# Kernel optimization log

Measured on AMD Instinct MI355X. Metric: run time of the kernel, lower is better.

Reference implementation:

```python
import jax, jax.numpy as jnp
import numpy as np

B, D_IN, D_PROJ, N_CLS = 4096, 4096, 1024, 32
N_CHILD = (32, 64)


def setup_inputs() -> dict:
    key = jax.random.key(0)
    ks = jax.random.split(key, 12)
    std = 2e-05
    inp = {
        "x": jax.random.normal(ks[0], (B, D_IN), dtype=jnp.float32),
        "y": jax.random.randint(ks[1], (B,), 0, N_CLS, dtype=jnp.int32),
        # parent projection: Linear(D_IN, D_PROJ)
        "Wp": jax.random.normal(ks[2], (D_IN, D_PROJ), dtype=jnp.float32) * std,
        "bp": jnp.zeros((D_PROJ,), jnp.float32),
        # subclass projection: Linear(D_IN, D_PROJ)
        "Ws": jax.random.normal(ks[3], (D_IN, D_PROJ), dtype=jnp.float32) * std,
        "bs": jnp.zeros((D_PROJ,), jnp.float32),
        # parent classifier: Linear(D_PROJ, N_CLS)
        "Wc": jax.random.normal(ks[4], (D_PROJ, N_CLS), dtype=jnp.float32) * std,
        "bc": jnp.zeros((N_CLS,), jnp.float32),
        # child expert banks: level i has N_CLS experts of Linear(D_PROJ, N_CHILD[i])
        "cw0": jax.random.normal(ks[5], (N_CLS, N_CHILD[0], D_PROJ), dtype=jnp.float32) * std,
        "cb0": jnp.zeros((N_CLS, N_CHILD[0]), jnp.float32),
        "cw1": jax.random.normal(ks[6], (N_CLS, N_CHILD[1], D_PROJ), dtype=jnp.float32) * std,
        "cb1": jnp.zeros((N_CLS, N_CHILD[1]), jnp.float32),
    }
    return inp


def reference(x, y, Wp, bp, Ws, bs, Wc, bc, cw0, cb0, cw1, cb1):
    # dropout p = 0.0 -> identity
    parent_proj_embed = x @ Wp + bp                 # [B, D_PROJ]
    parent_logits = parent_proj_embed @ Wc + bc     # [B, N_CLS]
    child_proj_embed = x @ Ws + bs                  # [B, D_PROJ]
    # per-sample expert routing: gather the expert for label y[b], then batched matvec
    child_logits0 = jnp.einsum("bd,bnd->bn", child_proj_embed, cw0[y]) + cb0[y]  # [B, 32]
    child_logits1 = jnp.einsum("bd,bnd->bn", child_proj_embed, cw1[y]) + cb1[y]  # [B, 64]
    return (parent_logits, child_logits0, child_logits1, parent_proj_embed, child_proj_embed)
```

## Files before the change

kernel.cpp:

```cpp
#include <hip/hip_runtime.h>
#include <hip/hip_bf16.h>
#include <stdint.h>


typedef __attribute__((ext_vector_type(4))) float  floatx4;
typedef __attribute__((ext_vector_type(8))) short  shortx8;
typedef __attribute__((ext_vector_type(4))) short  shortx4;
typedef __attribute__((ext_vector_type(8))) __bf16 bf16x8;

static __device__ __forceinline__ ushort f32_to_bf16_rne(float f) {
  uint32_t u = __builtin_bit_cast(uint32_t, f);
  u += 0x7FFFu + ((u >> 16) & 1u);
  return (ushort)(u >> 16);
}

static __device__ __forceinline__ void async_copy16(const void* g, void* lds) {
  __builtin_amdgcn_global_load_lds(
      (__attribute__((address_space(1))) void*)(uintptr_t)g,
      (__attribute__((address_space(3))) void*)(uintptr_t)lds,
      16, 0, 0);
}

__global__ __launch_bounds__(256) void k_prep(
    const float* __restrict__ x,   const int* __restrict__ y,
    const float* __restrict__ Wp,  const float* __restrict__ Ws,
    const float* __restrict__ Wc,
    const float* __restrict__ cw0, const float* __restrict__ cw1,
    ushort* __restrict__ xb,  ushort* __restrict__ Bt1,
    ushort* __restrict__ cwb, ushort* __restrict__ Wcb,
    int* __restrict__ perm, int* __restrict__ offs)
{
  __shared__ __align__(16) ushort tile[64 * 72];
  __shared__ int hist[32], hbase[32], hcur[32];
  const int b = blockIdx.x;
  const int t = threadIdx.x;

  if (b == 0) {
    if (t < 32) { hist[t] = 0; hcur[t] = 0; }
    __syncthreads();
    int yv[16];
    #pragma unroll
    for (int i = 0; i < 16; ++i) { yv[i] = y[t * 16 + i]; atomicAdd(&hist[yv[i]], 1); }
    __syncthreads();
    if (t == 0) {
      int s = 0;
      for (int c = 0; c < 32; ++c) { hbase[c] = s; offs[c] = s; s += hist[c]; }
      offs[32] = s;
    }
    __syncthreads();
    #pragma unroll
    for (int i = 0; i < 16; ++i) {
      const int c = yv[i];
      const int p = atomicAdd(&hcur[c], 1);
      perm[hbase[c] + p] = t * 16 + i;
    }
  } else if (b <= 4224) {
    const int row = b - 1;
    const int k = t * 4;
    float v0 = 0.f, v1 = 0.f, v2 = 0.f, v3 = 0.f;
    ushort* dst;
    if (row < 4096) {
      const int c = row >> 7, n = row & 127;
      if (n < 32) {
        floatx4 f = *reinterpret_cast<const floatx4*>(cw0 + (size_t)(c * 32 + n) * 1024 + k);
        v0 = f[0]; v1 = f[1]; v2 = f[2]; v3 = f[3];
      } else if (n < 96) {
        floatx4 f = *reinterpret_cast<const floatx4*>(cw1 + (size_t)(c * 64 + (n - 32)) * 1024 + k);
        v0 = f[0]; v1 = f[1]; v2 = f[2]; v3 = f[3];
      }
      dst = cwb + (size_t)row * 1024 + k;
    } else {
      const int n = row - 4096;
      if (n < 32) {
        v0 = Wc[(k + 0) * 32 + n]; v1 = Wc[(k + 1) * 32 + n];
        v2 = Wc[(k + 2) * 32 + n]; v3 = Wc[(k + 3) * 32 + n];
      }
      dst = Wcb + (size_t)n * 1024 + k;
    }
    shortx4 o;
    o[0] = (short)f32_to_bf16_rne(v0); o[1] = (short)f32_to_bf16_rne(v1);
    o[2] = (short)f32_to_bf16_rne(v2); o[3] = (short)f32_to_bf16_rne(v3);
    *reinterpret_cast<shortx4*>(dst) = o;
  } else if (b <= 6272) {
    const int vt = b - 4225;
    const int z = vt >> 10, rest = vt & 1023;
    const int nt = rest >> 6, kt = rest & 63;
    const float* W = z ? Ws : Wp;
    const int r = t >> 4, c = (t & 15) * 4;
    #pragma unroll
    for (int j = 0; j < 4; ++j) {
      const int kk = r + j * 16;
      floatx4 v = *reinterpret_cast<const floatx4*>(
          W + (size_t)(kt * 64 + kk) * 1024 + nt * 64 + c);
      tile[(c + 0) * 72 + kk] = f32_to_bf16_rne(v[0]);
      tile[(c + 1) * 72 + kk] = f32_to_bf16_rne(v[1]);
      tile[(c + 2) * 72 + kk] = f32_to_bf16_rne(v[2]);
      tile[(c + 3) * 72 + kk] = f32_to_bf16_rne(v[3]);
    }
    __syncthreads();
    const int nl = t >> 3, ch = t & 7;
    #pragma unroll
    for (int j = 0; j < 2; ++j) {
      const int n = nl + j * 32;
      shortx8 v = *reinterpret_cast<const shortx8*>(tile + n * 72 + ch * 8);
      *reinterpret_cast<shortx8*>(
          Bt1 + (size_t)(z * 1024 + nt * 64 + n) * 4096 + kt * 64 + ch * 8) = v;
    }
  } else {
    const size_t i = ((size_t)(b - 6273) * 256 + t) * 8;
    floatx4 a = *reinterpret_cast<const floatx4*>(x + i);
    floatx4 c = *reinterpret_cast<const floatx4*>(x + i + 4);
    shortx8 o;
    o[0] = (short)f32_to_bf16_rne(a[0]); o[1] = (short)f32_to_bf16_rne(a[1]);
    o[2] = (short)f32_to_bf16_rne(a[2]); o[3] = (short)f32_to_bf16_rne(a[3]);
    o[4] = (short)f32_to_bf16_rne(c[0]); o[5] = (short)f32_to_bf16_rne(c[1]);
    o[6] = (short)f32_to_bf16_rne(c[2]); o[7] = (short)f32_to_bf16_rne(c[3]);
    *reinterpret_cast<shortx8*>(xb + i) = o;
  }
}

__global__ __launch_bounds__(512, 2) void k_gemm1(
    const ushort* __restrict__ xb, const ushort* __restrict__ Bt1,
    const float* __restrict__ bp, const float* __restrict__ bs,
    float* __restrict__ outP, float* __restrict__ outS,
    ushort* __restrict__ Pb, ushort* __restrict__ Sb)
{
  __shared__ __align__(16) ushort lA[3 * 256 * 64];
  __shared__ __align__(16) ushort lB[3 * 128 * 64];

  floatx4 acc[4][4];
  const floatx4 z4 = {0.f, 0.f, 0.f, 0.f};
  #pragma unroll
  for (int i = 0; i < 4; ++i)
    #pragma unroll
    for (int j = 0; j < 4; ++j) acc[i][j] = z4;

  const int t    = threadIdx.x;
  const int w    = t >> 6;
  const int lane = t & 63;
  const int wr   = w >> 1;
  const int wc   = w & 1;
  const int r16  = lane & 15;
  const int qd   = lane >> 4;

  const ushort* Abase = xb  + (size_t)(blockIdx.x * 256) * 4096;
  const ushort* Bbase = Bt1 + (size_t)(blockIdx.y * 128) * 4096;

  const int    rS   = t >> 3;
  const int    qs   = ((t & 7) ^ (rS & 7)) << 3;
  const int    dUni = (t & ~63) * 8;

  const int px0 = (0 * 4 + qd) ^ (r16 & 7);
  const int px1 = (1 * 4 + qd) ^ (r16 & 7);
  const int aRd = (wr * 64 + r16) * 64;
  const int bRd = (wc * 64 + r16) * 64;

  #define STAGE_CHUNK(slot, k0)                                                \
    do {                                                                       \
      _Pragma("unroll")                                                        \
      for (int j = 0; j < 4; ++j)                                              \
        async_copy16(Abase + (size_t)(j * 64 + rS) * 4096 + (k0) + qs,         \
                     lA + (slot) * 16384 + j * 4096 + dUni);                   \
      _Pragma("unroll")                                                        \
      for (int j = 0; j < 2; ++j)                                              \
        async_copy16(Bbase + (size_t)(j * 64 + rS) * 4096 + (k0) + qs,         \
                     lB + (slot) * 8192 + j * 4096 + dUni);                    \
    } while (0)

  STAGE_CHUNK(0, 0);
  STAGE_CHUNK(1, 64);
  asm volatile("s_waitcnt vmcnt(6)" ::: "memory");
  __builtin_amdgcn_s_barrier();
  asm volatile("" ::: "memory");

  for (int c = 0; c < 64; ++c) {
    const int slot = c % 3;
    const ushort* As = lA + slot * 16384;
    const ushort* Bs = lB + slot * 8192;

    bf16x8 af[2][4], bfv[2][4];
    #pragma unroll
    for (int mi = 0; mi < 4; ++mi) {
      af[0][mi] = *reinterpret_cast<const bf16x8*>(As + aRd + mi * 1024 + px0 * 8);
      af[1][mi] = *reinterpret_cast<const bf16x8*>(As + aRd + mi * 1024 + px1 * 8);
    }
    #pragma unroll
    for (int ni = 0; ni < 4; ++ni) {
      bfv[0][ni] = *reinterpret_cast<const bf16x8*>(Bs + bRd + ni * 1024 + px0 * 8);
      bfv[1][ni] = *reinterpret_cast<const bf16x8*>(Bs + bRd + ni * 1024 + px1 * 8);
    }

    {
      const int cs  = c + 2;
      const int ss  = cs % 3;
      const int k0s = (cs < 64 ? cs : 63) * 64;
      STAGE_CHUNK(ss, k0s);
    }

    __builtin_amdgcn_s_setprio(1);
    #pragma unroll
    for (int ks = 0; ks < 2; ++ks)
      #pragma unroll
      for (int mi = 0; mi < 4; ++mi)
        #pragma unroll
        for (int ni = 0; ni < 4; ++ni)
          acc[mi][ni] = __builtin_amdgcn_mfma_f32_16x16x32_bf16(
              af[ks][mi], bfv[ks][ni], acc[mi][ni], 0, 0, 0);
    __builtin_amdgcn_s_setprio(0);

    asm volatile("s_waitcnt vmcnt(6)" ::: "memory");
    __builtin_amdgcn_s_barrier();
    asm volatile("" ::: "memory");
  }
  #undef STAGE_CHUNK

  const int sel = (blockIdx.y >= 8);
  const float* bias = sel ? bs : bp;
  float*  outF = sel ? outS : outP;
  ushort* outB = sel ? Sb : Pb;
  const int colbase = blockIdx.y * 128 - sel * 1024;
  #pragma unroll
  for (int mi = 0; mi < 4; ++mi) {
    #pragma unroll
    for (int ni = 0; ni < 4; ++ni) {
      const int n = colbase + wc * 64 + ni * 16 + r16;
      const float bv = bias[n];
      #pragma unroll
      for (int rg = 0; rg < 4; ++rg) {
        const int m = blockIdx.x * 256 + wr * 64 + mi * 16 + qd * 4 + rg;
        const float v = acc[mi][ni][rg] + bv;
        const size_t off = (size_t)m * 1024 + n;
        outF[off] = v;
        outB[off] = f32_to_bf16_rne(v);
      }
    }
  }
}

static __device__ __forceinline__ void load_frags64(
    const ushort* lA, const ushort* lB, bf16x8 af[2][4], bf16x8 bfv[2][4],
    int wr, int wc, int r16, int quad)
{
  #pragma unroll
  for (int ks = 0; ks < 2; ++ks) {
    const int pc = (((ks * 4) + quad) ^ (r16 & 7)) * 8;
    #pragma unroll
    for (int mi = 0; mi < 4; ++mi)
      af[ks][mi] = *reinterpret_cast<const bf16x8*>(lA + (wr * 64 + mi * 16 + r16) * 64 + pc);
    #pragma unroll
    for (int ni = 0; ni < 4; ++ni)
      bfv[ks][ni] = *reinterpret_cast<const bf16x8*>(lB + (wc * 64 + ni * 16 + r16) * 64 + pc);
  }
}

static __device__ __forceinline__ void mfma_frags64(
    bf16x8 af[2][4], bf16x8 bfv[2][4], floatx4 acc[4][4])
{
  __builtin_amdgcn_s_setprio(1);
  #pragma unroll
  for (int ks = 0; ks < 2; ++ks)
    #pragma unroll
    for (int mi = 0; mi < 4; ++mi)
      #pragma unroll
      for (int ni = 0; ni < 4; ++ni)
        acc[mi][ni] = __builtin_amdgcn_mfma_f32_16x16x32_bf16(
            af[ks][mi], bfv[ks][ni], acc[mi][ni], 0, 0, 0);
  __builtin_amdgcn_s_setprio(0);
}

__global__ __launch_bounds__(256) void k_head(
    const ushort* __restrict__ Sb, const ushort* __restrict__ Pb,
    const ushort* __restrict__ cwb, const ushort* __restrict__ Wcb,
    const int* __restrict__ perm, const int* __restrict__ off,
    const float* __restrict__ cb0, const float* __restrict__ cb1,
    const float* __restrict__ bc,
    float* __restrict__ out0, float* __restrict__ out1,
    float* __restrict__ outParent)
{
  __shared__ __align__(16) ushort lA[3 * 128 * 64];
  __shared__ __align__(16) ushort lB[3 * 128 * 64];
  floatx4 acc[4][4];
  const floatx4 z4 = {0.f, 0.f, 0.f, 0.f};
  #pragma unroll
  for (int i = 0; i < 4; ++i)
    #pragma unroll
    for (int j = 0; j < 4; ++j) acc[i][j] = z4;

  const int t = threadIdx.x, w = t >> 6, lane = t & 63;
  const int wr = w >> 1, wc = w & 1, r16 = lane & 15, quad = lane >> 4;
  const int sr = lane >> 3, sc = lane & 7;
  const int gc = sc ^ sr;
  const int dRow = 32 * w;

  if (blockIdx.x == 32) {
    const ushort* Abase = Pb + (size_t)(blockIdx.y * 128) * 1024;

    #define STAGE_P(slot, k0)                                                  \
      do {                                                                     \
        _Pragma("unroll")                                                      \
        for (int c2 = 0; c2 < 4; ++c2) {                                       \
          const int r = dRow + 8 * c2 + sr;                                    \
          async_copy16(Abase + (size_t)r * 1024 + (k0) + gc * 8,               \
                       lA + (slot) * 8192 + (dRow + 8 * c2) * 64);             \
          async_copy16(Wcb + (size_t)r * 1024 + (k0) + gc * 8,                 \
                       lB + (slot) * 8192 + (dRow + 8 * c2) * 64);             \
        }                                                                      \
      } while (0)

    STAGE_P(0, 0);
    STAGE_P(1, 64);
    asm volatile("s_waitcnt vmcnt(8)" ::: "memory");
    __builtin_amdgcn_s_barrier();
    asm volatile("" ::: "memory");

    for (int c = 0; c < 16; ++c) {
      const int slot = c % 3;
      bf16x8 af[2][4], bfv[2][4];
      load_frags64(lA + slot * 8192, lB + slot * 8192, af, bfv, wr, wc, r16, quad);
      {
        const int cs  = c + 2;
        const int ss  = cs % 3;
        const int k0s = (cs < 16 ? cs : 15) * 64;
        STAGE_P(ss, k0s);
      }
      mfma_frags64(af, bfv, acc);
      asm volatile("s_waitcnt vmcnt(8)" ::: "memory");
      __builtin_amdgcn_s_barrier();
      asm volatile("" ::: "memory");
    }
    #undef STAGE_P

    if (wc == 0) {
      #pragma unroll
      for (int mi = 0; mi < 4; ++mi)
        #pragma unroll
        for (int ni = 0; ni < 2; ++ni) {
          const int n = ni * 16 + r16;
          const float bv = bc[n];
          #pragma unroll
          for (int rg = 0; rg < 4; ++rg) {
            const int m = blockIdx.y * 128 + wr * 64 + mi * 16 + quad * 4 + rg;
            outParent[(size_t)m * 32 + n] = acc[mi][ni][rg] + bv;
          }
        }
    }
    return;
  }

  const int cls  = blockIdx.x;
  const int off0 = off[cls];
  const int cnt  = off[cls + 1] - off0;
  const int m0   = blockIdx.y * 128;
  if (m0 >= cnt) return;

  int rowSamp[4];
  #pragma unroll
  for (int c2 = 0; c2 < 4; ++c2) {
    const int r = dRow + 8 * c2 + sr;
    rowSamp[c2] = perm[off0 + min(m0 + r, cnt - 1)];
  }
  const ushort* Bbase = cwb + (size_t)cls * 128 * 1024;

  #define STAGE_C(slot, k0)                                                    \
    do {                                                                       \
      _Pragma("unroll")                                                        \
      for (int c2 = 0; c2 < 4; ++c2) {                                         \
        const int r = dRow + 8 * c2 + sr;                                      \
        async_copy16(Sb + (size_t)rowSamp[c2] * 1024 + (k0) + gc * 8,          \
                     lA + (slot) * 8192 + (dRow + 8 * c2) * 64);               \
        async_copy16(Bbase + (size_t)r * 1024 + (k0) + gc * 8,                 \
                     lB + (slot) * 8192 + (dRow + 8 * c2) * 64);               \
      }                                                                        \
    } while (0)

  STAGE_C(0, 0);
  STAGE_C(1, 64);
  asm volatile("s_waitcnt vmcnt(8)" ::: "memory");
  __builtin_amdgcn_s_barrier();
  asm volatile("" ::: "memory");

  for (int c = 0; c < 16; ++c) {
    const int slot = c % 3;
    bf16x8 af[2][4], bfv[2][4];
    load_frags64(lA + slot * 8192, lB + slot * 8192, af, bfv, wr, wc, r16, quad);
    {
      const int cs  = c + 2;
      const int ss  = cs % 3;
      const int k0s = (cs < 16 ? cs : 15) * 64;
      STAGE_C(ss, k0s);
    }
    mfma_frags64(af, bfv, acc);
    asm volatile("s_waitcnt vmcnt(8)" ::: "memory");
    __builtin_amdgcn_s_barrier();
    asm volatile("" ::: "memory");
  }
  #undef STAGE_C

  #pragma unroll
  for (int mi = 0; mi < 4; ++mi) {
    #pragma unroll
    for (int rg = 0; rg < 4; ++rg) {
      const int gm = m0 + wr * 64 + mi * 16 + quad * 4 + rg;
      if (gm >= cnt) continue;
      const int sample = perm[off0 + gm];
      #pragma unroll
      for (int ni = 0; ni < 4; ++ni) {
        const int n = wc * 64 + ni * 16 + r16;
        if (n < 32)
          out0[(size_t)sample * 32 + n] = acc[mi][ni][rg] + cb0[cls * 32 + n];
        else if (n < 96)
          out1[(size_t)sample * 64 + (n - 32)] = acc[mi][ni][rg] + cb1[cls * 64 + (n - 32)];
      }
    }
  }
}


extern "C" void kernel_launch(void* const* d_in, const int* in_sizes, int n_in,
                              void* d_out, int out_size, void* d_ws, size_t ws_size,
                              hipStream_t stream) {
  const float* x   = (const float*)d_in[0];
  const int*   y   = (const int*)  d_in[1];
  const float* Wp  = (const float*)d_in[2];
  const float* bp  = (const float*)d_in[3];
  const float* Ws  = (const float*)d_in[4];
  const float* bs  = (const float*)d_in[5];
  const float* Wc  = (const float*)d_in[6];
  const float* bc  = (const float*)d_in[7];
  const float* cw0 = (const float*)d_in[8];
  const float* cb0 = (const float*)d_in[9];
  const float* cw1 = (const float*)d_in[10];
  const float* cb1 = (const float*)d_in[11];

  float* out = (float*)d_out;
  float* parent_logits = out;
  float* child0        = out + 131072;
  float* child1        = out + 262144;
  float* P             = out + 524288;
  float* S             = out + 4718592;

  char* ws = (char*)d_ws;
  ushort* xb   = (ushort*)(ws);
  ushort* Bt1  = (ushort*)(ws + 33554432);
  ushort* Pb   = (ushort*)(ws + 50331648);
  ushort* Sb   = (ushort*)(ws + 58720256);
  ushort* cwb  = (ushort*)(ws + 67108864);
  ushort* Wcb  = (ushort*)(ws + 75497472);
  int*    perm = (int*)   (ws + 75759616);
  int*    offs = (int*)   (ws + 75776000);

  k_prep <<<14465, 256, 0, stream>>>(x, y, Wp, Ws, Wc, cw0, cw1,
                                     xb, Bt1, cwb, Wcb, perm, offs);
  k_gemm1<<<dim3(16, 16), 512, 0, stream>>>(xb, Bt1, bp, bs, P, S, Pb, Sb);
  k_head <<<dim3(33, 32), 256, 0, stream>>>(Sb, Pb, cwb, Wcb, perm, offs,
                                            cb0, cb1, bc,
                                            child0, child1, parent_logits);
}
```

Measured before the change: 252.5 us.

## Schedule head tiles via a compact work list with persistent blocks and deeper prefetch

k_prep now builds a list of real (class, M-tile) work items plus the parent-logit tiles. k_head launches 96 persistent blocks that loop over this list, instead of a 33x32 grid where most blocks exit early. The LDS ring grows from 3 to 4 stages, so loads are issued 3 chunks ahead. The aim is to cut empty-block launch overhead and hide more memory latency. The cost is 128KB of LDS per block and serial list construction on a single thread.

```diff
diff --git a/kernel.cpp b/kernel.cpp
--- a/kernel.cpp
+++ b/kernel.cpp
@@ -28,7 +28,8 @@
     const float* __restrict__ cw0, const float* __restrict__ cw1,
     ushort* __restrict__ xb,  ushort* __restrict__ Bt1,
     ushort* __restrict__ cwb, ushort* __restrict__ Wcb,
-    int* __restrict__ perm, int* __restrict__ offs)
+    int* __restrict__ perm, int* __restrict__ offs,
+    int* __restrict__ work, int* __restrict__ nwork)
 {
   __shared__ __align__(16) ushort tile[64 * 72];
   __shared__ int hist[32], hbase[32], hcur[32];
@@ -46,6 +47,11 @@
       int s = 0;
       for (int c = 0; c < 32; ++c) { hbase[c] = s; offs[c] = s; s += hist[c]; }
       offs[32] = s;
+      int nw = 0;
+      for (int m = 0; m < 32; ++m) work[nw++] = (32 << 8) | m;
+      for (int c = 0; c < 32; ++c)
+        for (int m0 = 0; m0 < hist[c]; m0 += 128) work[nw++] = (c << 8) | (m0 >> 7);
+      nwork[0] = nw;
     }
     __syncthreads();
     #pragma unroll
@@ -272,144 +278,123 @@
     const ushort* __restrict__ Sb, const ushort* __restrict__ Pb,
     const ushort* __restrict__ cwb, const ushort* __restrict__ Wcb,
     const int* __restrict__ perm, const int* __restrict__ off,
+    const int* __restrict__ work, const int* __restrict__ nwork,
     const float* __restrict__ cb0, const float* __restrict__ cb1,
     const float* __restrict__ bc,
     float* __restrict__ out0, float* __restrict__ out1,
     float* __restrict__ outParent)
 {
-  __shared__ __align__(16) ushort lA[3 * 128 * 64];
-  __shared__ __align__(16) ushort lB[3 * 128 * 64];
-  floatx4 acc[4][4];
-  const floatx4 z4 = {0.f, 0.f, 0.f, 0.f};
-  #pragma unroll
-  for (int i = 0; i < 4; ++i)
-    #pragma unroll
-    for (int j = 0; j < 4; ++j) acc[i][j] = z4;
+  __shared__ __align__(16) ushort lA[4 * 128 * 64];
+  __shared__ __align__(16) ushort lB[4 * 128 * 64];
 
   const int t = threadIdx.x, w = t >> 6, lane = t & 63;
   const int wr = w >> 1, wc = w & 1, r16 = lane & 15, quad = lane >> 4;
   const int sr = lane >> 3, sc = lane & 7;
   const int gc = sc ^ sr;
   const int dRow = 32 * w;
-
-  if (blockIdx.x == 32) {
-    const ushort* Abase = Pb + (size_t)(blockIdx.y * 128) * 1024;
-
-    #define STAGE_P(slot, k0)                                                  \
+  const int nW = nwork[0];
+
+  for (int wi = blockIdx.x; wi < nW; wi += 96) {
+    const int item = work[wi];
+    const int cls  = item >> 8;
+    const int mt   = item & 255;
+
+    floatx4 acc[4][4];
+    const floatx4 z4 = {0.f, 0.f, 0.f, 0.f};
+    #pragma unroll
+    for (int i = 0; i < 4; ++i)
+      #pragma unroll
+      for (int j = 0; j < 4; ++j) acc[i][j] = z4;
+
+    int off0 = 0, cnt = 0;
+    const ushort* Asrc;
+    const ushort* Bb;
+    int rowG[4];
+    if (cls == 32) {
+      Asrc = Pb;
+      Bb   = Wcb;
+      #pragma unroll
+      for (int c2 = 0; c2 < 4; ++c2) rowG[c2] = mt * 128 + dRow + 8 * c2 + sr;
+    } else {
+      off0 = off[cls];
+      cnt  = off[cls + 1] - off0;
+      Asrc = Sb;
+      Bb   = cwb + (size_t)cls * 128 * 1024;
+      #pragma unroll
+      for (int c2 = 0; c2 < 4; ++c2) {
+        const int r = mt * 128 + dRow + 8 * c2 + sr;
+        rowG[c2] = perm[off0 + min(r, cnt - 1)];
+      }
+    }
+
+    #define STAGE_H(slot, k0)                                                  \
       do {                                                                     \
         _Pragma("unroll")                                                      \
         for (int c2 = 0; c2 < 4; ++c2) {                                       \
-          const int r = dRow + 8 * c2 + sr;                                    \
-          async_copy16(Abase + (size_t)r * 1024 + (k0) + gc * 8,               \
+          async_copy16(Asrc + (size_t)rowG[c2] * 1024 + (k0) + gc * 8,         \
                        lA + (slot) * 8192 + (dRow + 8 * c2) * 64);             \
-          async_copy16(Wcb + (size_t)r * 1024 + (k0) + gc * 8,                 \
+          async_copy16(Bb + (size_t)(dRow + 8 * c2 + sr) * 1024 + (k0) + gc * 8,\
                        lB + (slot) * 8192 + (dRow + 8 * c2) * 64);             \
         }                                                                      \
       } while (0)
 
-    STAGE_P(0, 0);
-    STAGE_P(1, 64);
-    asm volatile("s_waitcnt vmcnt(8)" ::: "memory");
+    STAGE_H(0, 0);
+    STAGE_H(1, 64);
+    STAGE_H(2, 128);
+    asm volatile("s_waitcnt vmcnt(16)" ::: "memory");
     __builtin_amdgcn_s_barrier();
     asm volatile("" ::: "memory");
 
     for (int c = 0; c < 16; ++c) {
-      const int slot = c % 3;
+      const int slot = c & 3;
       bf16x8 af[2][4], bfv[2][4];
       load_frags64(lA + slot * 8192, lB + slot * 8192, af, bfv, wr, wc, r16, quad);
       {
-        const int cs  = c + 2;
-        const int ss  = cs % 3;
+        const int cs  = c + 3;
+        const int ss  = cs & 3;
         const int k0s = (cs < 16 ? cs : 15) * 64;
-        STAGE_P(ss, k0s);
+        STAGE_H(ss, k0s);
       }
       mfma_frags64(af, bfv, acc);
-      asm volatile("s_waitcnt vmcnt(8)" ::: "memory");
+      asm volatile("s_waitcnt vmcnt(16)" ::: "memory");
       __builtin_amdgcn_s_barrier();
       asm volatile("" ::: "memory");
     }
-    #undef STAGE_P
-
-    if (wc == 0) {
-      #pragma unroll
-      for (int mi = 0; mi < 4; ++mi)
+    #undef STAGE_H
+
+    if (cls == 32) {
+      if (wc == 0) {
         #pragma unroll
-        for (int ni = 0; ni < 2; ++ni) {
-          const int n = ni * 16 + r16;
-          const float bv = bc[n];
+        for (int mi = 0; mi < 4; ++mi)
           #pragma unroll
-          for (int rg = 0; rg < 4; ++rg) {
-            const int m = blockIdx.y * 128 + wr * 64 + mi * 16 + quad * 4 + rg;
-            outParent[(size_t)m * 32 + n] = acc[mi][ni][rg] + bv;
+          for (int ni = 0; ni < 2; ++ni) {
+            const int n = ni * 16 + r16;
+            const float bv = bc[n];
+            #pragma unroll
+            for (int rg = 0; rg < 4; ++rg) {
+              const int m = mt * 128 + wr * 64 + mi * 16 + quad * 4 + rg;
+              outParent[(size_t)m * 32 + n] = acc[mi][ni][rg] + bv;
+            }
+          }
+      }
+    } else {
+      const int m0 = mt * 128;
+      #pragma unroll
+      for (int mi = 0; mi < 4; ++mi) {
+        #pragma unroll
+        for (int rg = 0; rg < 4; ++rg) {
+          const int gm = m0 + wr * 64 + mi * 16 + quad * 4 + rg;
+          if (gm >= cnt) continue;
+          const int sample = perm[off0 + gm];
+          #pragma unroll
+          for (int ni = 0; ni < 4; ++ni) {
+            const int n = wc * 64 + ni * 16 + r16;
+            if (n < 32)
+              out0[(size_t)sample * 32 + n] = acc[mi][ni][rg] + cb0[cls * 32 + n];
+            else if (n < 96)
+              out1[(size_t)sample * 64 + (n - 32)] = acc[mi][ni][rg] + cb1[cls * 64 + (n - 32)];
           }
         }
-    }
-    return;
-  }
-
-  const int cls  = blockIdx.x;
-  const int off0 = off[cls];
-  const int cnt  = off[cls + 1] - off0;
-  const int m0   = blockIdx.y * 128;
-  if (m0 >= cnt) return;
-
-  int rowSamp[4];
-  #pragma unroll
-  for (int c2 = 0; c2 < 4; ++c2) {
-    const int r = dRow + 8 * c2 + sr;
-    rowSamp[c2] = perm[off0 + min(m0 + r, cnt - 1)];
-  }
-  const ushort* Bbase = cwb + (size_t)cls * 128 * 1024;
-
-  #define STAGE_C(slot, k0)                                                    \
-    do {                                                                       \
-      _Pragma("unroll")                                                        \
-      for (int c2 = 0; c2 < 4; ++c2) {                                         \
-        const int r = dRow + 8 * c2 + sr;                                      \
-        async_copy16(Sb + (size_t)rowSamp[c2] * 1024 + (k0) + gc * 8,          \
-                     lA + (slot) * 8192 + (dRow + 8 * c2) * 64);               \
-        async_copy16(Bbase + (size_t)r * 1024 + (k0) + gc * 8,                 \
-                     lB + (slot) * 8192 + (dRow + 8 * c2) * 64);               \
-      }                                                                        \
-    } while (0)
-
-  STAGE_C(0, 0);
-  STAGE_C(1, 64);
-  asm volatile("s_waitcnt vmcnt(8)" ::: "memory");
-  __builtin_amdgcn_s_barrier();
-  asm volatile("" ::: "memory");
-
-  for (int c = 0; c < 16; ++c) {
-    const int slot = c % 3;
-    bf16x8 af[2][4], bfv[2][4];
-    load_frags64(lA + slot * 8192, lB + slot * 8192, af, bfv, wr, wc, r16, quad);
-    {
-      const int cs  = c + 2;
-      const int ss  = cs % 3;
-      const int k0s = (cs < 16 ? cs : 15) * 64;
-      STAGE_C(ss, k0s);
-    }
-    mfma_frags64(af, bfv, acc);
-    asm volatile("s_waitcnt vmcnt(8)" ::: "memory");
-    __builtin_amdgcn_s_barrier();
-    asm volatile("" ::: "memory");
-  }
-  #undef STAGE_C
-
-  #pragma unroll
-  for (int mi = 0; mi < 4; ++mi) {
-    #pragma unroll
-    for (int rg = 0; rg < 4; ++rg) {
-      const int gm = m0 + wr * 64 + mi * 16 + quad * 4 + rg;
-      if (gm >= cnt) continue;
-      const int sample = perm[off0 + gm];
-      #pragma unroll
-      for (int ni = 0; ni < 4; ++ni) {
-        const int n = wc * 64 + ni * 16 + r16;
-        if (n < 32)
-          out0[(size_t)sample * 32 + n] = acc[mi][ni][rg] + cb0[cls * 32 + n];
-        else if (n < 96)
-          out1[(size_t)sample * 64 + (n - 32)] = acc[mi][ni][rg] + cb1[cls * 64 + (n - 32)];
       }
     }
   }
@@ -448,11 +433,13 @@
   ushort* Wcb  = (ushort*)(ws + 75497472);
   int*    perm = (int*)   (ws + 75759616);
   int*    offs = (int*)   (ws + 75776000);
+  int*    work = (int*)   (ws + 75776256);
+  int*    nwk  = (int*)   (ws + 75776768);
 
   k_prep <<<14465, 256, 0, stream>>>(x, y, Wp, Ws, Wc, cw0, cw1,
-                                     xb, Bt1, cwb, Wcb, perm, offs);
+                                     xb, Bt1, cwb, Wcb, perm, offs, work, nwk);
   k_gemm1<<<dim3(16, 16), 512, 0, stream>>>(xb, Bt1, bp, bs, P, S, Pb, Sb);
-  k_head <<<dim3(33, 32), 256, 0, stream>>>(Sb, Pb, cwb, Wcb, perm, offs,
-                                            cb0, cb1, bc,
-                                            child0, child1, parent_logits);
-}
+  k_head <<<96, 256, 0, stream>>>(Sb, Pb, cwb, Wcb, perm, offs, work, nwk,
+                                  cb0, cb1, bc,
+                                  child0, child1, parent_logits);
+}
```

Measured after the change: 248.2 us. Within noise of the previous version (-1.7%).
